# Kernel optimization log

Measured on AMD Instinct MI355X. Metric: run time of the kernel, lower is better.

Reference implementation:

```python
import jax, jax.numpy as jnp
import numpy as np

N_NODES = 20000
N_EDGES = 200000
N_GRAPHS = 500
F = 512      # num_features
H = 512      # hidden_dim
C = 10       # num_classes
K = 30       # sort-pool k


def setup_inputs() -> dict:
    key = jax.random.key(0)
    ks = jax.random.split(key, 12)
    p = lambda k, shp: (jax.random.normal(k, shp, jnp.float32) * 0.05)
    x = jax.random.normal(ks[0], (N_NODES, F), jnp.float32)
    edge_index = jax.random.randint(ks[1], (2, N_EDGES), 0, N_NODES, dtype=jnp.int32)
    batch = jnp.sort(jax.random.randint(ks[2], (N_NODES,), 0, N_GRAPHS, dtype=jnp.int32))
    return dict(
        x=x, edge_index=edge_index, batch=batch,
        W1=p(ks[3], (F, H)), b1=jnp.zeros((H,), jnp.float32),
        W2=p(ks[4], (H, H)), b2=jnp.zeros((H,), jnp.float32),
        W3=p(ks[5], (H, 1)), b3=jnp.zeros((1,), jnp.float32),
        cw1=p(ks[6], (16, 1, 2 * H + 1)), cb1=jnp.zeros((16,), jnp.float32),
        cw2=p(ks[7], (32, 16, 5)), cb2=jnp.zeros((32,), jnp.float32),
        lw1=p(ks[8], (352, H)), lb1=jnp.zeros((H,), jnp.float32),
        lw2=p(ks[9], (H, C)), lb2=jnp.zeros((C,), jnp.float32),
    )


def gcn_conv(x, W, b, src, dst):
    # PyG GCNConv: add self-loops, symmetric deg^-1/2 normalization, then scatter-add.
    n = x.shape[0]
    loop = jnp.arange(n, dtype=src.dtype)
    s = jnp.concatenate([src, loop])
    d = jnp.concatenate([dst, loop])
    deg = jax.ops.segment_sum(jnp.ones_like(d, dtype=x.dtype), d, num_segments=n)
    dinv = jnp.where(deg > 0, jax.lax.rsqrt(deg), 0.0)
    norm = dinv[s] * dinv[d]                       # [E+N]
    h = x @ W                                      # transform first (in < out ok)
    out = jax.ops.segment_sum(h[s] * norm[:, None], d, num_segments=n)
    return out + b


def global_sort_pool(feat, batch, num_graphs, k):
    # Sort nodes within each graph by last feature channel (descending),
    # keep first k per graph, zero-pad short graphs. Returns [G, k*D].
    n, D = feat.shape
    key = feat[:, -1]
    order = jnp.lexsort((-key, batch))             # primary: batch asc, secondary: key desc
    bs = batch[order]
    fs = feat[order]
    counts = jax.ops.segment_sum(jnp.ones_like(batch, dtype=jnp.int32), batch, num_segments=num_graphs)
    starts = jnp.cumsum(counts) - counts
    rank = jnp.arange(n, dtype=jnp.int32) - starts[bs]
    valid = rank < k
    pooled = jnp.zeros((num_graphs, k, D), feat.dtype).at[
        bs, jnp.clip(rank, 0, k - 1)
    ].add(jnp.where(valid[:, None], fs, 0.0))
    return pooled.reshape(num_graphs, k * D)


def reference(x, edge_index, batch, W1, b1, W2, b2, W3, b3,
              cw1, cb1, cw2, cb2, lw1, lb1, lw2, lb2):
    src, dst = edge_index[0], edge_index[1]
    x1 = jax.nn.elu(gcn_conv(x, W1, b1, src, dst))                 # dropout = identity (eval)
    x2 = jax.nn.elu(gcn_conv(x1, W2, b2, src, dst) + x1)
    out = gcn_conv(x2, W3, b3, src, dst)                           # [N, 1]
    feat = jnp.concatenate([x1, x2, out], axis=-1)                 # [N, 2H+1]
    D = feat.shape[-1]
    z = global_sort_pool(feat, batch, N_GRAPHS, K)                 # [G, K*D]
    z = z[:, None, :]                                              # [G, 1, K*D]
    dn = ('NCH', 'OIH', 'NCH')
    z = jax.nn.relu(jax.lax.conv_general_dilated(z, cw1, (D,), 'VALID', dimension_numbers=dn) + cb1[None, :, None])  # [G,16,30]
    z = jax.lax.reduce_window(z, -jnp.inf, jax.lax.max, (1, 1, 2), (1, 1, 2), 'VALID')                               # [G,16,15]
    z = jax.nn.relu(jax.lax.conv_general_dilated(z, cw2, (1,), 'VALID', dimension_numbers=dn) + cb2[None, :, None])  # [G,32,11]
    z = z.reshape(z.shape[0], -1)                                  # [G,352]
    z = jax.nn.relu(z @ lw1 + lb1)
    return z @ lw2 + lb2                                           # [G, C]
```

## Files before the change

### kernel.cpp

```cpp
#include <hip/hip_runtime.h>
#include <hip/hip_bf16.h>

#define NN 20000
#define NEDGE 200000
#define NG 500
#define KTOP 30
#define HDIM 512


__global__ void k_init(int* indeg, int* ccur, int* gcnt) {
    int i = blockIdx.x * 256 + threadIdx.x;
    if (i < NN) { indeg[i] = 0; ccur[i] = 0; }
    if (i < NG) gcnt[i] = 0;
}

__global__ void k_count(const int* __restrict__ dst, int* indeg, int ne) {
    int e = blockIdx.x * 256 + threadIdx.x;
    if (e < ne) atomicAdd(&indeg[dst[e]], 1);
}

__global__ void k_gcount(const int* __restrict__ batch, int* gcnt) {
    int i = blockIdx.x * 256 + threadIdx.x;
    if (i < NN) atomicAdd(&gcnt[batch[i]], 1);
}

__global__ void k_dinv(const int* __restrict__ indeg, float* dinv) {
    int i = blockIdx.x * 256 + threadIdx.x;
    if (i < NN) dinv[i] = rsqrtf((float)(indeg[i] + 1));
}

__global__ void k_scan(const int* __restrict__ in, int* __restrict__ out, int n) {
    const int NT = 256;
    __shared__ int sums[NT];
    int t = threadIdx.x;
    int per = (n + NT - 1) / NT;
    int s0 = t * per;
    int local = 0;
    for (int k = 0; k < per; ++k) { int idx = s0 + k; if (idx < n) local += in[idx]; }
    sums[t] = local;
    __syncthreads();
    for (int off = 1; off < NT; off <<= 1) {
        int v = (t >= off) ? sums[t - off] : 0;
        __syncthreads();
        sums[t] += v;
        __syncthreads();
    }
    int run = sums[t] - local;
    for (int k = 0; k < per; ++k) { int idx = s0 + k; if (idx < n) { out[idx] = run; run += in[idx]; } }
    if (t == NT - 1) out[n] = run;
}

__global__ void k_fill(const int* __restrict__ src, const int* __restrict__ dst,
                       const int* __restrict__ cstart, int* ccur, int* csrc, int ne) {
    int e = blockIdx.x * 256 + threadIdx.x;
    if (e < ne) {
        int d = dst[e];
        int pos = cstart[d] + atomicAdd(&ccur[d], 1);
        csrc[pos] = src[e];
    }
}


__global__ __launch_bounds__(256) void k_gemm(const float* __restrict__ A, const float* __restrict__ B,
                                              float* __restrict__ C, int M) {
    const int K = 512, N = 512;
    __shared__ float As[8][128];
    __shared__ float Bs[8][128];
    int t = threadIdx.x;
    int bm = blockIdx.x * 128, bn = blockIdx.y * 128;
    int tm = t >> 4, tn = t & 15;
    float acc[8][8];
    #pragma unroll
    for (int i = 0; i < 8; ++i)
        #pragma unroll
        for (int j = 0; j < 8; ++j) acc[i][j] = 0.f;

    int arow = t >> 1, acol = (t & 1) * 4;
    int brow = t >> 5, bcol = (t & 31) * 4;
    int arow_c = min(bm + arow, M - 1);
    const float* Aptr = A + (size_t)arow_c * K + acol;
    const float* Bptr = B + (size_t)brow * N + bn + bcol;

    float4 av = *(const float4*)(Aptr);
    float4 bv = *(const float4*)(Bptr);

    for (int k0 = 0; k0 < K; k0 += 8) {
        As[acol + 0][arow] = av.x;
        As[acol + 1][arow] = av.y;
        As[acol + 2][arow] = av.z;
        As[acol + 3][arow] = av.w;
        *(float4*)&Bs[brow][bcol] = bv;
        __syncthreads();
        if (k0 + 8 < K) {
            av = *(const float4*)(Aptr + k0 + 8);
            bv = *(const float4*)(Bptr + (size_t)(k0 + 8) * N);
        }
        #pragma unroll
        for (int kk = 0; kk < 8; ++kk) {
            float a[8], b[8];
            #pragma unroll
            for (int i = 0; i < 8; ++i) a[i] = As[kk][tm * 8 + i];
            #pragma unroll
            for (int j = 0; j < 8; ++j) b[j] = Bs[kk][tn * 8 + j];
            #pragma unroll
            for (int i = 0; i < 8; ++i)
                #pragma unroll
                for (int j = 0; j < 8; ++j)
                    acc[i][j] = fmaf(a[i], b[j], acc[i][j]);
        }
        __syncthreads();
    }
    #pragma unroll
    for (int i = 0; i < 8; ++i) {
        int r = bm + tm * 8 + i;
        if (r < M) {
            float4 v0 = make_float4(acc[i][0], acc[i][1], acc[i][2], acc[i][3]);
            float4 v1 = make_float4(acc[i][4], acc[i][5], acc[i][6], acc[i][7]);
            *(float4*)(C + (size_t)r * N + bn + tn * 8)     = v0;
            *(float4*)(C + (size_t)r * N + bn + tn * 8 + 4) = v1;
        }
    }
}


__global__ __launch_bounds__(256) void k_agg(const float* __restrict__ h, const int* __restrict__ cstart,
                                             const int* __restrict__ csrc, const float* __restrict__ dinv,
                                             const float* __restrict__ bias, const float* __restrict__ res,
                                             float* __restrict__ out) {
    int w = blockIdx.x * 4 + (threadIdx.x >> 6);
    if (w >= NN) return;
    int lane = threadIdx.x & 63;
    float di = dinv[w];
    float acc[8] = {0, 0, 0, 0, 0, 0, 0, 0};
    int e0 = cstart[w], e1 = cstart[w + 1];
    for (int j = e0; j < e1; ++j) {
        int s = csrc[j];
        float wt = dinv[s] * di;
        const float* hr = h + (size_t)s * HDIM + lane * 8;
        float4 v0 = *(const float4*)hr;
        float4 v1 = *(const float4*)(hr + 4);
        acc[0] = fmaf(v0.x, wt, acc[0]); acc[1] = fmaf(v0.y, wt, acc[1]);
        acc[2] = fmaf(v0.z, wt, acc[2]); acc[3] = fmaf(v0.w, wt, acc[3]);
        acc[4] = fmaf(v1.x, wt, acc[4]); acc[5] = fmaf(v1.y, wt, acc[5]);
        acc[6] = fmaf(v1.z, wt, acc[6]); acc[7] = fmaf(v1.w, wt, acc[7]);
    }
    {
        float wt = di * di;
        const float* hr = h + (size_t)w * HDIM + lane * 8;
        float4 v0 = *(const float4*)hr;
        float4 v1 = *(const float4*)(hr + 4);
        acc[0] = fmaf(v0.x, wt, acc[0]); acc[1] = fmaf(v0.y, wt, acc[1]);
        acc[2] = fmaf(v0.z, wt, acc[2]); acc[3] = fmaf(v0.w, wt, acc[3]);
        acc[4] = fmaf(v1.x, wt, acc[4]); acc[5] = fmaf(v1.y, wt, acc[5]);
        acc[6] = fmaf(v1.z, wt, acc[6]); acc[7] = fmaf(v1.w, wt, acc[7]);
    }
    const float* bptr = bias + lane * 8;
    const float* rptr = res ? res + (size_t)w * HDIM + lane * 8 : nullptr;
    float v[8];
    #pragma unroll
    for (int q = 0; q < 8; ++q) {
        float t = acc[q] + bptr[q];
        if (rptr) t += rptr[q];
        v[q] = t > 0.f ? t : (expf(t) - 1.f);
    }
    float* orow = out + (size_t)w * HDIM + lane * 8;
    *(float4*)orow       = make_float4(v[0], v[1], v[2], v[3]);
    *(float4*)(orow + 4) = make_float4(v[4], v[5], v[6], v[7]);
}


__global__ __launch_bounds__(256) void k_gemv3(const float* __restrict__ x2, const float* __restrict__ W3,
                                               float* __restrict__ h3) {
    int w = blockIdx.x * 4 + (threadIdx.x >> 6);
    if (w >= NN) return;
    int lane = threadIdx.x & 63;
    const float* r = x2 + (size_t)w * HDIM + lane * 8;
    const float* wp = W3 + lane * 8;
    float4 a0 = *(const float4*)r, a1 = *(const float4*)(r + 4);
    float4 w0 = *(const float4*)wp, w1 = *(const float4*)(wp + 4);
    float acc = a0.x * w0.x + a0.y * w0.y + a0.z * w0.z + a0.w * w0.w
              + a1.x * w1.x + a1.y * w1.y + a1.z * w1.z + a1.w * w1.w;
    #pragma unroll
    for (int off = 32; off; off >>= 1) acc += __shfl_down(acc, off);
    if (lane == 0) h3[w] = acc;
}

__global__ void k_agg3(const float* __restrict__ h3, const int* __restrict__ cstart,
                       const int* __restrict__ csrc, const float* __restrict__ dinv,
                       const float* __restrict__ b3, float* __restrict__ key) {
    int i = blockIdx.x * 256 + threadIdx.x;
    if (i >= NN) return;
    float di = dinv[i];
    float acc = h3[i] * di * di;
    int e0 = cstart[i], e1 = cstart[i + 1];
    for (int j = e0; j < e1; ++j) {
        int s = csrc[j];
        acc = fmaf(h3[s], dinv[s] * di, acc);
    }
    key[i] = acc + b3[0];
}


#define MAXN 2048
__global__ __launch_bounds__(256) void k_select(const float* __restrict__ key, const int* __restrict__ gstart,
                                                int* __restrict__ sel) {
    int g = blockIdx.x;
    int s = gstart[g], e = gstart[g + 1];
    int cnt = e - s;
    if (cnt > MAXN) cnt = MAXN;
    __shared__ float ks[MAXN];
    __shared__ int sels[KTOP];
    for (int i = threadIdx.x; i < cnt; i += 256) ks[i] = key[s + i];
    if (threadIdx.x < KTOP) sels[threadIdx.x] = -1;
    __syncthreads();
    for (int i = threadIdx.x; i < cnt; i += 256) {
        float ki = ks[i];
        int r = 0;
        for (int j = 0; j < cnt; ++j) {
            float kj = ks[j];
            r += (kj > ki) || (kj == ki && j < i);
        }
        if (r < KTOP) sels[r] = s + i;
    }
    __syncthreads();
    if (threadIdx.x < KTOP) sel[g * KTOP + threadIdx.x] = sels[threadIdx.x];
}


__global__ __launch_bounds__(256) void k_conv1(const float* __restrict__ x1, const float* __restrict__ x2,
                                               const float* __restrict__ key, const int* __restrict__ sel,
                                               const float* __restrict__ cw1, const float* __restrict__ cb1,
                                               float* __restrict__ c1) {
    int gp = blockIdx.x;
    int g = gp / KTOP, p = gp - g * KTOP;
    int t = threadIdx.x;
    int node = sel[gp];
    if (node < 0) {
        if (t < 16) c1[((size_t)g * 16 + t) * KTOP + p] = fmaxf(cb1[t], 0.f);
        return;
    }
    __shared__ float f[1025];
    __shared__ float red[16][17];
    if (t < 128) {
        ((float4*)f)[t] = ((const float4*)(x1 + (size_t)node * HDIM))[t];
    } else {
        ((float4*)(f + 512))[t - 128] = ((const float4*)(x2 + (size_t)node * HDIM))[t - 128];
    }
    if (t == 0) f[1024] = key[node];
    __syncthreads();
    int oc = t >> 4, ch = t & 15;
    const float* wrow = cw1 + (size_t)oc * 1025;
    float pd = 0.f;
    for (int k = ch; k < 1025; k += 16) pd = fmaf(f[k], wrow[k], pd);
    red[oc][ch] = pd;
    __syncthreads();
    if (t < 16) {
        float ssum = cb1[t];
        #pragma unroll
        for (int c = 0; c < 16; ++c) ssum += red[t][c];
        c1[((size_t)g * 16 + t) * KTOP + p] = fmaxf(ssum, 0.f);
    }
}


__global__ __launch_bounds__(512) void k_head(const float* __restrict__ c1, const float* __restrict__ cw2,
                                              const float* __restrict__ cb2, const float* __restrict__ lw1,
                                              const float* __restrict__ lb1, const float* __restrict__ lw2,
                                              const float* __restrict__ lb2, float* __restrict__ outp) {
    int g = blockIdx.x, t = threadIdx.x;
    __shared__ float m[16][15];
    __shared__ float z2s[352];
    __shared__ float z3[512];
    if (t < 240) {
        int ic = t / 15, q = t % 15;
        const float* row = c1 + ((size_t)g * 16 + ic) * KTOP;
        m[ic][q] = fmaxf(row[2 * q], row[2 * q + 1]);
    }
    __syncthreads();
    if (t < 352) {
        int oc = t / 11, tt = t % 11;
        float acc = cb2[oc];
        #pragma unroll
        for (int ic = 0; ic < 16; ++ic)
            #pragma unroll
            for (int j = 0; j < 5; ++j)
                acc = fmaf(m[ic][tt + j], cw2[((size_t)oc * 16 + ic) * 5 + j], acc);
        z2s[t] = fmaxf(acc, 0.f);
    }
    __syncthreads();
    {
        float acc = lb1[t];
        for (int k = 0; k < 352; ++k) acc = fmaf(z2s[k], lw1[(size_t)k * 512 + t], acc);
        z3[t] = fmaxf(acc, 0.f);
    }
    __syncthreads();
    if (t < 160) {
        int oc = t >> 4, l = t & 15;
        float acc = 0.f;
        for (int k = l; k < 512; k += 16) acc = fmaf(z3[k], lw2[(size_t)k * 10 + oc], acc);
        #pragma unroll
        for (int off = 1; off < 16; off <<= 1) acc += __shfl_xor(acc, off);
        if (l == 0) outp[g * 10 + oc] = acc + lb2[oc];
    }
}


extern "C" void kernel_launch(void* const* d_in, const int* in_sizes, int n_in,
                              void* d_out, int out_size, void* d_ws, size_t ws_size,
                              hipStream_t stream) {
    const float* x    = (const float*)d_in[0];
    const int*   ei   = (const int*)d_in[1];
    const int*   batch= (const int*)d_in[2];
    const float* W1   = (const float*)d_in[3];
    const float* b1   = (const float*)d_in[4];
    const float* W2   = (const float*)d_in[5];
    const float* b2   = (const float*)d_in[6];
    const float* W3   = (const float*)d_in[7];
    const float* b3   = (const float*)d_in[8];
    const float* cw1  = (const float*)d_in[9];
    const float* cb1  = (const float*)d_in[10];
    const float* cw2  = (const float*)d_in[11];
    const float* cb2  = (const float*)d_in[12];
    const float* lw1  = (const float*)d_in[13];
    const float* lb1  = (const float*)d_in[14];
    const float* lw2  = (const float*)d_in[15];
    const float* lb2  = (const float*)d_in[16];

    const int NE = in_sizes[1] / 2;
    const int* srcp = ei;
    const int* dstp = ei + NE;

    char* ws = (char*)d_ws;
    size_t o = 0;
    auto al = [&](size_t b) { size_t r = o; o += (b + 255) & ~(size_t)255; return r; };
    int*   indeg  = (int*)(ws + al((size_t)NN * 4));
    int*   ccur   = (int*)(ws + al((size_t)NN * 4));
    int*   cstart = (int*)(ws + al((size_t)(NN + 1) * 4));
    int*   csrc   = (int*)(ws + al((size_t)NE * 4));
    float* dinv   = (float*)(ws + al((size_t)NN * 4));
    float* h      = (float*)(ws + al((size_t)NN * HDIM * 4));
    float* x1     = (float*)(ws + al((size_t)NN * HDIM * 4));
    float* x2     = (float*)(ws + al((size_t)NN * HDIM * 4));
    float* h3     = (float*)(ws + al((size_t)NN * 4));
    float* key    = (float*)(ws + al((size_t)NN * 4));
    int*   gcnt   = (int*)(ws + al((size_t)NG * 4));
    int*   gstart = (int*)(ws + al((size_t)(NG + 1) * 4));
    int*   sel    = (int*)(ws + al((size_t)NG * KTOP * 4));
    float* c1     = (float*)(ws + al((size_t)NG * 16 * KTOP * 4));
    (void)ws_size; (void)n_in; (void)out_size;

    int nb_n = (NN + 255) / 256;
    int nb_e = (NE + 255) / 256;

    k_init<<<nb_n, 256, 0, stream>>>(indeg, ccur, gcnt);
    k_count<<<nb_e, 256, 0, stream>>>(dstp, indeg, NE);
    k_gcount<<<nb_n, 256, 0, stream>>>(batch, gcnt);
    k_dinv<<<nb_n, 256, 0, stream>>>(indeg, dinv);
    k_scan<<<1, 256, 0, stream>>>(indeg, cstart, NN);
    k_scan<<<1, 256, 0, stream>>>(gcnt, gstart, NG);
    k_fill<<<nb_e, 256, 0, stream>>>(srcp, dstp, cstart, ccur, csrc, NE);

    dim3 gg((NN + 127) / 128, 4);
    k_gemm<<<gg, 256, 0, stream>>>(x, W1, h, NN);
    k_agg<<<NN / 4, 256, 0, stream>>>(h, cstart, csrc, dinv, b1, nullptr, x1);
    k_gemm<<<gg, 256, 0, stream>>>(x1, W2, h, NN);
    k_agg<<<NN / 4, 256, 0, stream>>>(h, cstart, csrc, dinv, b2, x1, x2);
    k_gemv3<<<NN / 4, 256, 0, stream>>>(x2, W3, h3);
    k_agg3<<<nb_n, 256, 0, stream>>>(h3, cstart, csrc, dinv, b3, key);

    k_select<<<NG, 256, 0, stream>>>(key, gstart, sel);
    k_conv1<<<NG * KTOP, 256, 0, stream>>>(x1, x2, key, sel, cw1, cb1, c1);
    k_head<<<NG, 512, 0, stream>>>(c1, cw2, cb2, lw1, lb1, lw2, lb2, (float*)d_out);
}
```

Measured before the change: 746.5 us.

## Replace FP32 SIMT GEMMs with split-bf16 MFMA GEMMs (3-term emulation)

New measurement: 684.0 us. 1.09x faster.

```diff
diff --git a/kernel.cpp b/kernel.cpp
--- a/kernel.cpp
+++ b/kernel.cpp
@@ -6,6 +6,17 @@
 #define NG 500
 #define KTOP 30
 #define HDIM 512
+
+typedef __attribute__((ext_vector_type(8))) short s16x8;
+typedef __attribute__((ext_vector_type(4))) float f32x4;
+
+__device__ __forceinline__ unsigned short f2bf(float f) {
+    unsigned int u = __float_as_uint(f);
+    return (unsigned short)((u + 0x7FFFu + ((u >> 16) & 1u)) >> 16);
+}
+__device__ __forceinline__ float bf2f(unsigned short s) {
+    return __uint_as_float(((unsigned int)s) << 16);
+}
 
 
 __global__ void k_init(int* indeg, int* ccur, int* gcnt) {
@@ -61,65 +72,144 @@
 }
 
 
-__global__ __launch_bounds__(256) void k_gemm(const float* __restrict__ A, const float* __restrict__ B,
-                                              float* __restrict__ C, int M) {
-    const int K = 512, N = 512;
-    __shared__ float As[8][128];
-    __shared__ float Bs[8][128];
-    int t = threadIdx.x;
-    int bm = blockIdx.x * 128, bn = blockIdx.y * 128;
-    int tm = t >> 4, tn = t & 15;
-    float acc[8][8];
-    #pragma unroll
-    for (int i = 0; i < 8; ++i)
-        #pragma unroll
-        for (int j = 0; j < 8; ++j) acc[i][j] = 0.f;
-
-    int arow = t >> 1, acol = (t & 1) * 4;
-    int brow = t >> 5, bcol = (t & 31) * 4;
-    int arow_c = min(bm + arow, M - 1);
-    const float* Aptr = A + (size_t)arow_c * K + acol;
-    const float* Bptr = B + (size_t)brow * N + bn + bcol;
-
-    float4 av = *(const float4*)(Aptr);
-    float4 bv = *(const float4*)(Bptr);
-
-    for (int k0 = 0; k0 < K; k0 += 8) {
-        As[acol + 0][arow] = av.x;
-        As[acol + 1][arow] = av.y;
-        As[acol + 2][arow] = av.z;
-        As[acol + 3][arow] = av.w;
-        *(float4*)&Bs[brow][bcol] = bv;
+__global__ __launch_bounds__(256) void k_split(const float* __restrict__ A,
+                                               unsigned short* __restrict__ o0,
+                                               unsigned short* __restrict__ o1,
+                                               unsigned short* __restrict__ o2, int n4) {
+    int i = blockIdx.x * 256 + threadIdx.x;
+    if (i >= n4) return;
+    float4 v = ((const float4*)A)[i];
+    float f[4] = {v.x, v.y, v.z, v.w};
+    unsigned short h0[4], h1[4], h2[4];
+    #pragma unroll
+    for (int j = 0; j < 4; ++j) {
+        h0[j] = f2bf(f[j]);   float r = f[j] - bf2f(h0[j]);
+        h1[j] = f2bf(r);      r -= bf2f(h1[j]);
+        h2[j] = f2bf(r);
+    }
+    ((ushort4*)o0)[i] = make_ushort4(h0[0], h0[1], h0[2], h0[3]);
+    ((ushort4*)o1)[i] = make_ushort4(h1[0], h1[1], h1[2], h1[3]);
+    ((ushort4*)o2)[i] = make_ushort4(h2[0], h2[1], h2[2], h2[3]);
+}
+
+__global__ __launch_bounds__(256) void k_splitW(const float* __restrict__ W,
+                                                unsigned short* __restrict__ w0,
+                                                unsigned short* __restrict__ w1,
+                                                unsigned short* __restrict__ w2) {
+    __shared__ float tile[32][33];
+    int bk = blockIdx.x * 32, bn = blockIdx.y * 32;
+    int tx = threadIdx.x & 31, ty = threadIdx.x >> 5;
+    #pragma unroll
+    for (int r = 0; r < 4; ++r)
+        tile[ty * 4 + r][tx] = W[(size_t)(bk + ty * 4 + r) * 512 + bn + tx];
+    __syncthreads();
+    #pragma unroll
+    for (int r = 0; r < 4; ++r) {
+        int n = bn + ty * 4 + r, k = bk + tx;
+        float v = tile[tx][ty * 4 + r];
+        unsigned short a0 = f2bf(v); float rr = v - bf2f(a0);
+        unsigned short a1 = f2bf(rr); rr -= bf2f(a1);
+        w0[(size_t)n * 512 + k] = a0;
+        w1[(size_t)n * 512 + k] = a1;
+        w2[(size_t)n * 512 + k] = f2bf(rr);
+    }
+}
+
+
+#define ASTR (NN * HDIM)
+#define BSTR (512 * 512)
+
+__global__ __launch_bounds__(256) void k_gemm_mfma(const unsigned short* __restrict__ S,
+                                                   const unsigned short* __restrict__ Wt,
+                                                   float* __restrict__ C, int M) {
+    __shared__ short lds[6][4096];
+    const int t = threadIdx.x;
+    const int lane = t & 63, wid = t >> 6;
+    const int wr = wid >> 1, wc = wid & 1;
+    const int bm = blockIdx.x * 128, bn = blockIdx.y * 128;
+    const int arow = lane & 15, koff = (lane >> 4) * 8;
+
+    int offA[6], offB[6], ldsA[6], ldsB[6];
+    #pragma unroll
+    for (int i = 0; i < 6; ++i) {
+        int u = i * 4 + wid;
+        int c = u >> 3, g = u & 7;
+        int row = bm + g * 16 + arow; if (row >= M) row = M - 1;
+        offA[i] = c * ASTR + row * HDIM + koff;
+        ldsA[i] = c * 4096 + (g * 64 + lane) * 8;
+    }
+    #pragma unroll
+    for (int i = 0; i < 6; ++i) {
+        int u = i * 4 + wid;
+        int c = u >> 3, g = u & 7;
+        int row = bn + g * 16 + arow;
+        offB[i] = c * BSTR + row * 512 + koff;
+        ldsB[i] = (3 + c) * 4096 + (g * 64 + lane) * 8;
+    }
+
+    f32x4 acc[4][4];
+    #pragma unroll
+    for (int m = 0; m < 4; ++m)
+        #pragma unroll
+        for (int n = 0; n < 4; ++n) acc[m][n] = (f32x4){0.f, 0.f, 0.f, 0.f};
+
+    s16x8 stA[6], stB[6];
+    #pragma unroll
+    for (int i = 0; i < 6; ++i) stA[i] = *(const s16x8*)(S + offA[i]);
+    #pragma unroll
+    for (int i = 0; i < 6; ++i) stB[i] = *(const s16x8*)(Wt + offB[i]);
+
+    short* lp = &lds[0][0];
+    #pragma unroll 1
+    for (int s = 0; s < 16; ++s) {
         __syncthreads();
-        if (k0 + 8 < K) {
-            av = *(const float4*)(Aptr + k0 + 8);
-            bv = *(const float4*)(Bptr + (size_t)(k0 + 8) * N);
-        }
-        #pragma unroll
-        for (int kk = 0; kk < 8; ++kk) {
-            float a[8], b[8];
-            #pragma unroll
-            for (int i = 0; i < 8; ++i) a[i] = As[kk][tm * 8 + i];
-            #pragma unroll
-            for (int j = 0; j < 8; ++j) b[j] = Bs[kk][tn * 8 + j];
-            #pragma unroll
-            for (int i = 0; i < 8; ++i)
-                #pragma unroll
-                for (int j = 0; j < 8; ++j)
-                    acc[i][j] = fmaf(a[i], b[j], acc[i][j]);
+        #pragma unroll
+        for (int i = 0; i < 6; ++i) *(s16x8*)(lp + ldsA[i]) = stA[i];
+        #pragma unroll
+        for (int i = 0; i < 6; ++i) *(s16x8*)(lp + ldsB[i]) = stB[i];
+        if (s + 1 < 16) {
+            int kadv = (s + 1) * 32;
+            #pragma unroll
+            for (int i = 0; i < 6; ++i) stA[i] = *(const s16x8*)(S + offA[i] + kadv);
+            #pragma unroll
+            for (int i = 0; i < 6; ++i) stB[i] = *(const s16x8*)(Wt + offB[i] + kadv);
         }
         __syncthreads();
-    }
-    #pragma unroll
-    for (int i = 0; i < 8; ++i) {
-        int r = bm + tm * 8 + i;
-        if (r < M) {
-            float4 v0 = make_float4(acc[i][0], acc[i][1], acc[i][2], acc[i][3]);
-            float4 v1 = make_float4(acc[i][4], acc[i][5], acc[i][6], acc[i][7]);
-            *(float4*)(C + (size_t)r * N + bn + tn * 8)     = v0;
-            *(float4*)(C + (size_t)r * N + bn + tn * 8 + 4) = v1;
-        }
-    }
+        s16x8 af[3][4], bf[3][4];
+        #pragma unroll
+        for (int c = 0; c < 3; ++c)
+            #pragma unroll
+            for (int m = 0; m < 4; ++m)
+                af[c][m] = *(const s16x8*)(lp + c * 4096 + ((wr * 4 + m) * 64 + lane) * 8);
+        #pragma unroll
+        for (int c = 0; c < 3; ++c)
+            #pragma unroll
+            for (int n = 0; n < 4; ++n)
+                bf[c][n] = *(const s16x8*)(lp + (3 + c) * 4096 + ((wc * 4 + n) * 64 + lane) * 8);
+        #pragma unroll
+        for (int m = 0; m < 4; ++m)
+            #pragma unroll
+            for (int n = 0; n < 4; ++n) {
+                acc[m][n] = __builtin_amdgcn_mfma_f32_16x16x32_bf16(af[0][m], bf[0][n], acc[m][n], 0, 0, 0);
+                acc[m][n] = __builtin_amdgcn_mfma_f32_16x16x32_bf16(af[0][m], bf[1][n], acc[m][n], 0, 0, 0);
+                acc[m][n] = __builtin_amdgcn_mfma_f32_16x16x32_bf16(af[1][m], bf[0][n], acc[m][n], 0, 0, 0);
+                acc[m][n] = __builtin_amdgcn_mfma_f32_16x16x32_bf16(af[0][m], bf[2][n], acc[m][n], 0, 0, 0);
+                acc[m][n] = __builtin_amdgcn_mfma_f32_16x16x32_bf16(af[1][m], bf[1][n], acc[m][n], 0, 0, 0);
+                acc[m][n] = __builtin_amdgcn_mfma_f32_16x16x32_bf16(af[2][m], bf[0][n], acc[m][n], 0, 0, 0);
+            }
+    }
+
+    int crow0 = bm + wr * 64 + (lane >> 4) * 4;
+    int ccol0 = bn + wc * 64 + (lane & 15);
+    #pragma unroll
+    for (int m = 0; m < 4; ++m)
+        #pragma unroll
+        for (int n = 0; n < 4; ++n)
+            #pragma unroll
+            for (int r = 0; r < 4; ++r) {
+                int row = crow0 + m * 16 + r;
+                if (row < M) C[(size_t)row * 512 + ccol0 + n * 16] = acc[m][n][r];
+            }
 }
 
 
@@ -340,13 +430,15 @@
     float* dinv   = (float*)(ws + al((size_t)NN * 4));
     float* h      = (float*)(ws + al((size_t)NN * HDIM * 4));
     float* x1     = (float*)(ws + al((size_t)NN * HDIM * 4));
-    float* x2     = (float*)(ws + al((size_t)NN * HDIM * 4));
     float* h3     = (float*)(ws + al((size_t)NN * 4));
     float* key    = (float*)(ws + al((size_t)NN * 4));
     int*   gcnt   = (int*)(ws + al((size_t)NG * 4));
     int*   gstart = (int*)(ws + al((size_t)(NG + 1) * 4));
     int*   sel    = (int*)(ws + al((size_t)NG * KTOP * 4));
     float* c1     = (float*)(ws + al((size_t)NG * 16 * KTOP * 4));
+    unsigned short* S  = (unsigned short*)(ws + al((size_t)3 * NN * HDIM * 2));
+    unsigned short* Wt = (unsigned short*)(ws + al((size_t)3 * 512 * 512 * 2));
+    float* x2 = (float*)S;
     (void)ws_size; (void)n_in; (void)out_size;
 
     int nb_n = (NN + 255) / 256;
@@ -360,14 +452,21 @@
     k_scan<<<1, 256, 0, stream>>>(gcnt, gstart, NG);
     k_fill<<<nb_e, 256, 0, stream>>>(srcp, dstp, cstart, ccur, csrc, NE);
 
+    const int n4 = NN * HDIM / 4;
+    const int nsp = (n4 + 255) / 256;
+    dim3 gw(16, 16);
     dim3 gg((NN + 127) / 128, 4);
-    k_gemm<<<gg, 256, 0, stream>>>(x, W1, h, NN);
+
+    k_split<<<nsp, 256, 0, stream>>>(x, S, S + (size_t)NN * HDIM, S + (size_t)2 * NN * HDIM, n4);
+    k_splitW<<<gw, 256, 0, stream>>>(W1, Wt, Wt + 512 * 512, Wt + 2 * 512 * 512);
+    k_gemm_mfma<<<gg, 256, 0, stream>>>(S, Wt, h, NN);
     k_agg<<<NN / 4, 256, 0, stream>>>(h, cstart, csrc, dinv, b1, nullptr, x1);
-    k_gemm<<<gg, 256, 0, stream>>>(x1, W2, h, NN);
+    k_split<<<nsp, 256, 0, stream>>>(x1, S, S + (size_t)NN * HDIM, S + (size_t)2 * NN * HDIM, n4);
+    k_splitW<<<gw, 256, 0, stream>>>(W2, Wt, Wt + 512 * 512, Wt + 2 * 512 * 512);
+    k_gemm_mfma<<<gg, 256, 0, stream>>>(S, Wt, h, NN);
     k_agg<<<NN / 4, 256, 0, stream>>>(h, cstart, csrc, dinv, b2, x1, x2);
     k_gemv3<<<NN / 4, 256, 0, stream>>>(x2, W3, h3);
     k_agg3<<<nb_n, 256, 0, stream>>>(h3, cstart, csrc, dinv, b3, key);
-
     k_select<<<NG, 256, 0, stream>>>(key, gstart, sel);
     k_conv1<<<NG * KTOP, 256, 0, stream>>>(x1, x2, key, sel, cw1, cb1, c1);
     k_head<<<NG, 512, 0, stream>>>(c1, cw2, cb2, lw1, lb1, lw2, lb2, (float*)d_out);
```
